# Optimization experiments

Measured on AMD Instinct MI355X. Metric: run time of the kernel, lower is better.

Reference implementation:

```python
import jax, jax.numpy as jnp
import numpy as np

MEM = 2048

def _linear_params(key, scale):
    kw, kb = jax.random.split(key)
    W = jax.random.uniform(kw, (MEM, MEM), jnp.float32, -scale, scale)
    b = jax.random.uniform(kb, (MEM,), jnp.float32, -scale, scale)
    return W, b

def setup_inputs() -> dict:
    key = jax.random.key(0)
    ks = jax.random.split(key, 18)
    scale = 1.0 / np.sqrt(MEM)
    inp = {
        'lc': jax.random.normal(ks[0], (1, MEM), jnp.float32),
        'lh': jax.random.normal(ks[1], (1, MEM), jnp.float32),
        'rc': jax.random.normal(ks[2], (1, MEM), jnp.float32),
        'rh': jax.random.normal(ks[3], (1, MEM), jnp.float32),
        'S': jax.random.normal(ks[4], (1, MEM), jnp.float32),
        'w': jax.random.normal(ks[5], (1, MEM), jnp.float32),
    }
    names = ['Wh', 'Us', 'ma', 'ilh', 'irh', 'lflh', 'lfrh', 'rflh', 'rfrh', 'ulh', 'urh']
    for i, n in enumerate(names):
        W, b = _linear_params(ks[6 + i], scale)
        inp[n + '_w'] = W
        inp[n + '_b'] = b
    return inp

def _lin(x, W, b):
    return x @ W.T + b

def reference(lc, lh, rc, rh, S, w,
              Wh_w, Wh_b, Us_w, Us_b, ma_w, ma_b,
              ilh_w, ilh_b, irh_w, irh_b,
              lflh_w, lflh_b, lfrh_w, lfrh_b,
              rflh_w, rflh_b, rfrh_w, rfrh_b,
              ulh_w, ulh_b, urh_w, urh_b):
    # attention scoring over the two children
    m_left = jnp.tanh(_lin(lh, Wh_w, Wh_b) + _lin(S, Us_w, Us_b)).squeeze()   # [MEM]
    m_right = jnp.tanh(_lin(rh, Wh_w, Wh_b) + _lin(S, Us_w, Us_b)).squeeze()  # [MEM]
    exp_left = w @ m_left[:, None]    # [1,1]
    exp_right = w @ m_right[:, None]  # [1,1]
    denom = exp_left + exp_right
    left_alpha = exp_left / denom
    right_alpha = exp_right / denom
    # attention-weighted child hidden states
    la = jnp.tanh(_lin(left_alpha * lh, ma_w, ma_b))   # [1,MEM]
    ra = jnp.tanh(_lin(right_alpha * rh, ma_w, ma_b))  # [1,MEM]
    # tree-LSTM gates
    i = jax.nn.sigmoid(_lin(la, ilh_w, ilh_b) + _lin(ra, irh_w, irh_b))
    lf = jax.nn.sigmoid(_lin(la, lflh_w, lflh_b) + _lin(ra, lfrh_w, lfrh_b))
    rf = jax.nn.sigmoid(_lin(la, rflh_w, rflh_b) + _lin(ra, rfrh_w, rfrh_b))
    update = jnp.tanh(_lin(la, ulh_w, ulh_b) + _lin(ra, urh_w, urh_b))
    c = i * update + lf * lc + rf * rc
    h = jnp.tanh(c)
    return (c, h)
```

## Files before the change

### kernel.cpp

```cpp
#include <hip/hip_runtime.h>
#include <hip/hip_bf16.h>
#include <math.h>

#define MEM 2048
#define NT  256
#define NF4 (MEM / 4)

__device__ __forceinline__ float dot4(float4 a, float4 b) {
    return a.x * b.x + a.y * b.y + a.z * b.z + a.w * b.w;
}

__device__ __forceinline__ float wave_reduce(float v) {
#pragma unroll
    for (int off = 32; off > 0; off >>= 1)
        v += __shfl_down(v, off, 64);
    return v;
}

__device__ __forceinline__ float sigmoidf_(float x) {
    return 1.0f / (1.0f + expf(-x));
}

__global__ __launch_bounds__(NT) void
k1_score(const float* __restrict__ lh, const float* __restrict__ rh,
         const float* __restrict__ S,  const float* __restrict__ w,
         const float* __restrict__ Wh_w, const float* __restrict__ Wh_b,
         const float* __restrict__ Us_w, const float* __restrict__ Us_b,
         const float* __restrict__ ma_w,
         float* __restrict__ pl, float* __restrict__ pr,
         float* __restrict__ wml, float* __restrict__ wmr)
{
    __shared__ float s_red[4][5];

    const int t   = threadIdx.x;
    const int row = blockIdx.x;

    const float4* __restrict__ wh4 = (const float4*)(Wh_w + (size_t)row * MEM);
    const float4* __restrict__ us4 = (const float4*)(Us_w + (size_t)row * MEM);
    const float4* __restrict__ ma4 = (const float4*)(ma_w + (size_t)row * MEM);
    const float4* __restrict__ l4  = (const float4*)lh;
    const float4* __restrict__ r4  = (const float4*)rh;
    const float4* __restrict__ s4  = (const float4*)S;

    float awl = 0.f, awr = 0.f, aus = 0.f, aml = 0.f, amr = 0.f;
#pragma unroll
    for (int h = 0; h < 2; ++h) {
        const int i = t + h * NT;
        const float4 a  = wh4[i];
        const float4 u  = us4[i];
        const float4 m  = ma4[i];
        const float4 xl = l4[i];
        const float4 xr = r4[i];
        const float4 xs = s4[i];
        awl += dot4(a, xl);
        awr += dot4(a, xr);
        aus += dot4(u, xs);
        aml += dot4(m, xl);
        amr += dot4(m, xr);
    }
    awl = wave_reduce(awl);
    awr = wave_reduce(awr);
    aus = wave_reduce(aus);
    aml = wave_reduce(aml);
    amr = wave_reduce(amr);

    const int wv = t >> 6, ln = t & 63;
    if (ln == 0) {
        s_red[wv][0] = awl; s_red[wv][1] = awr; s_red[wv][2] = aus;
        s_red[wv][3] = aml; s_red[wv][4] = amr;
    }
    __syncthreads();
    if (t == 0) {
        float r0 = 0.f, r1 = 0.f, r2 = 0.f, r3 = 0.f, r4v = 0.f;
#pragma unroll
        for (int k = 0; k < 4; ++k) {
            r0 += s_red[k][0]; r1 += s_red[k][1]; r2 += s_red[k][2];
            r3 += s_red[k][3]; r4v += s_red[k][4];
        }
        const float us = r2 + Us_b[row];
        const float ml = tanhf(r0 + Wh_b[row] + us);
        const float mr = tanhf(r1 + Wh_b[row] + us);
        pl[row] = r3;
        pr[row] = r4v;
        const float wj = w[row];
        wml[row] = wj * ml;
        wmr[row] = wj * mr;
    }
}

__global__ __launch_bounds__(NT) void
k2_gates(const float* __restrict__ lc, const float* __restrict__ rc,
         const float* __restrict__ pl, const float* __restrict__ pr,
         const float* __restrict__ wml, const float* __restrict__ wmr,
         const float* __restrict__ ma_b,
         const float* __restrict__ ilh_w,  const float* __restrict__ ilh_b,
         const float* __restrict__ irh_w,  const float* __restrict__ irh_b,
         const float* __restrict__ lflh_w, const float* __restrict__ lflh_b,
         const float* __restrict__ lfrh_w, const float* __restrict__ lfrh_b,
         const float* __restrict__ rflh_w, const float* __restrict__ rflh_b,
         const float* __restrict__ rfrh_w, const float* __restrict__ rfrh_b,
         const float* __restrict__ ulh_w,  const float* __restrict__ ulh_b,
         const float* __restrict__ urh_w,  const float* __restrict__ urh_b,
         float* __restrict__ out)
{
    __shared__ __align__(16) float s_la[MEM];
    __shared__ __align__(16) float s_ra[MEM];
    __shared__ float s_red[4][4];
    __shared__ float s_al[2];

    const int t   = threadIdx.x;
    const int wv  = t >> 6, ln = t & 63;
    const int row = blockIdx.x;

    {
        const float4* __restrict__ wl4 = (const float4*)wml;
        const float4* __restrict__ wr4 = (const float4*)wmr;
        const float4 a0 = wl4[t], a1 = wl4[t + NT];
        const float4 b0 = wr4[t], b1 = wr4[t + NT];
        float el = a0.x + a0.y + a0.z + a0.w + a1.x + a1.y + a1.z + a1.w;
        float er = b0.x + b0.y + b0.z + b0.w + b1.x + b1.y + b1.z + b1.w;
        el = wave_reduce(el);
        er = wave_reduce(er);
        if (ln == 0) { s_red[wv][0] = el; s_red[wv][1] = er; }
    }
    __syncthreads();
    if (t == 0) {
        const float el = s_red[0][0] + s_red[1][0] + s_red[2][0] + s_red[3][0];
        const float er = s_red[0][1] + s_red[1][1] + s_red[2][1] + s_red[3][1];
        const float d  = el + er;
        s_al[0] = el / d;
        s_al[1] = er / d;
    }
    __syncthreads();
    const float al = s_al[0];
    const float ar = s_al[1];

    {
        const float4* __restrict__ p4 = (const float4*)pl;
        const float4* __restrict__ q4 = (const float4*)pr;
        const float4* __restrict__ b4 = (const float4*)ma_b;
        float4* sla4 = (float4*)s_la;
        float4* sra4 = (float4*)s_ra;
#pragma unroll
        for (int h = 0; h < 2; ++h) {
            const int i = t + h * NT;
            const float4 p = p4[i];
            const float4 q = q4[i];
            const float4 b = b4[i];
            float4 la, ra;
            la.x = tanhf(al * p.x + b.x); ra.x = tanhf(ar * q.x + b.x);
            la.y = tanhf(al * p.y + b.y); ra.y = tanhf(ar * q.y + b.y);
            la.z = tanhf(al * p.z + b.z); ra.z = tanhf(ar * q.z + b.z);
            la.w = tanhf(al * p.w + b.w); ra.w = tanhf(ar * q.w + b.w);
            sla4[i] = la;
            sra4[i] = ra;
        }
    }
    __syncthreads();

    const size_t off = (size_t)row * MEM;
    const float4* __restrict__ il4  = (const float4*)(ilh_w  + off);
    const float4* __restrict__ ir4  = (const float4*)(irh_w  + off);
    const float4* __restrict__ lfl4 = (const float4*)(lflh_w + off);
    const float4* __restrict__ lfr4 = (const float4*)(lfrh_w + off);
    const float4* __restrict__ rfl4 = (const float4*)(rflh_w + off);
    const float4* __restrict__ rfr4 = (const float4*)(rfrh_w + off);
    const float4* __restrict__ ul4  = (const float4*)(ulh_w  + off);
    const float4* __restrict__ ur4  = (const float4*)(urh_w  + off);
    const float4* sla4 = (const float4*)s_la;
    const float4* sra4 = (const float4*)s_ra;

    float gi = 0.f, glf = 0.f, grf = 0.f, gu = 0.f;
#pragma unroll
    for (int h = 0; h < 2; ++h) {
        const int i = t + h * NT;
        const float4 w0 = il4[i];
        const float4 w1 = ir4[i];
        const float4 w2 = lfl4[i];
        const float4 w3 = lfr4[i];
        const float4 w4 = rfl4[i];
        const float4 w5 = rfr4[i];
        const float4 w6 = ul4[i];
        const float4 w7 = ur4[i];
        const float4 xa = sla4[i];
        const float4 xb = sra4[i];
        gi  += dot4(w0, xa) + dot4(w1, xb);
        glf += dot4(w2, xa) + dot4(w3, xb);
        grf += dot4(w4, xa) + dot4(w5, xb);
        gu  += dot4(w6, xa) + dot4(w7, xb);
    }
    gi  = wave_reduce(gi);
    glf = wave_reduce(glf);
    grf = wave_reduce(grf);
    gu  = wave_reduce(gu);
    if (ln == 0) {
        s_red[wv][0] = gi; s_red[wv][1] = glf; s_red[wv][2] = grf; s_red[wv][3] = gu;
    }
    __syncthreads();
    if (t == 0) {
        float r0 = 0.f, r1 = 0.f, r2 = 0.f, r3 = 0.f;
#pragma unroll
        for (int k = 0; k < 4; ++k) {
            r0 += s_red[k][0]; r1 += s_red[k][1];
            r2 += s_red[k][2]; r3 += s_red[k][3];
        }
        const float ig  = sigmoidf_(r0 + ilh_b[row]  + irh_b[row]);
        const float lfg = sigmoidf_(r1 + lflh_b[row] + lfrh_b[row]);
        const float rfg = sigmoidf_(r2 + rflh_b[row] + rfrh_b[row]);
        const float ug  = tanhf(r3 + ulh_b[row] + urh_b[row]);
        const float c   = ig * ug + lfg * lc[row] + rfg * rc[row];
        out[row]       = c;
        out[MEM + row] = tanhf(c);
    }
}

extern "C" void kernel_launch(void* const* d_in, const int* in_sizes, int n_in,
                              void* d_out, int out_size, void* d_ws, size_t ws_size,
                              hipStream_t stream) {
    const float* lc = (const float*)d_in[0];
    const float* lh = (const float*)d_in[1];
    const float* rc = (const float*)d_in[2];
    const float* rh = (const float*)d_in[3];
    const float* S  = (const float*)d_in[4];
    const float* w  = (const float*)d_in[5];
    const float* Wh_w   = (const float*)d_in[6];   const float* Wh_b   = (const float*)d_in[7];
    const float* Us_w   = (const float*)d_in[8];   const float* Us_b   = (const float*)d_in[9];
    const float* ma_w   = (const float*)d_in[10];  const float* ma_b   = (const float*)d_in[11];
    const float* ilh_w  = (const float*)d_in[12];  const float* ilh_b  = (const float*)d_in[13];
    const float* irh_w  = (const float*)d_in[14];  const float* irh_b  = (const float*)d_in[15];
    const float* lflh_w = (const float*)d_in[16];  const float* lflh_b = (const float*)d_in[17];
    const float* lfrh_w = (const float*)d_in[18];  const float* lfrh_b = (const float*)d_in[19];
    const float* rflh_w = (const float*)d_in[20];  const float* rflh_b = (const float*)d_in[21];
    const float* rfrh_w = (const float*)d_in[22];  const float* rfrh_b = (const float*)d_in[23];
    const float* ulh_w  = (const float*)d_in[24];  const float* ulh_b  = (const float*)d_in[25];
    const float* urh_w  = (const float*)d_in[26];  const float* urh_b  = (const float*)d_in[27];

    float* out = (float*)d_out;
    float* ws  = (float*)d_ws;
    float* pl  = ws;
    float* pr  = ws + MEM;
    float* wml = ws + 2 * MEM;
    float* wmr = ws + 3 * MEM;

    k1_score<<<MEM, NT, 0, stream>>>(lh, rh, S, w, Wh_w, Wh_b, Us_w, Us_b,
                                     ma_w, pl, pr, wml, wmr);

    k2_gates<<<MEM, NT, 0, stream>>>(lc, rc, pl, pr, wml, wmr, ma_b,
                                     ilh_w, ilh_b, irh_w, irh_b,
                                     lflh_w, lflh_b, lfrh_w, lfrh_b,
                                     rflh_w, rflh_b, rfrh_w, rfrh_b,
                                     ulh_w, ulh_b, urh_w, urh_b, out);
}
```

Baseline: 244.0 us.

## Split GEMVs into per-matrix slab kernels with wave-per-two-rows mapping

Replaces the two row-per-block kernels with four kernels. Two slab GEMV kernels give each matrix its own grid dimension and assign two rows per wave, staging the input vector in shared memory. A single-block kernel now computes the attention alphas and la/ra once instead of recomputing them in every block of the gate kernel, and a final elementwise kernel combines the gates. This is meant to cut redundant per-block work and spread the weight streaming across more independent blocks, at the cost of two extra launches and a serial single-block step.

```diff
diff --git a/kernel.cpp b/kernel.cpp
--- a/kernel.cpp
+++ b/kernel.cpp
@@ -3,8 +3,7 @@
 #include <math.h>
 
 #define MEM 2048
-#define NT  256
-#define NF4 (MEM / 4)
+#define NF4 512
 
 __device__ __forceinline__ float dot4(float4 a, float4 b) {
     return a.x * b.x + a.y * b.y + a.z * b.z + a.w * b.w;
@@ -21,197 +20,179 @@
     return 1.0f / (1.0f + expf(-x));
 }
 
-__global__ __launch_bounds__(NT) void
-k1_score(const float* __restrict__ lh, const float* __restrict__ rh,
-         const float* __restrict__ S,  const float* __restrict__ w,
-         const float* __restrict__ Wh_w, const float* __restrict__ Wh_b,
-         const float* __restrict__ Us_w, const float* __restrict__ Us_b,
-         const float* __restrict__ ma_w,
-         float* __restrict__ pl, float* __restrict__ pr,
-         float* __restrict__ wml, float* __restrict__ wmr)
-{
-    __shared__ float s_red[4][5];
-
-    const int t   = threadIdx.x;
-    const int row = blockIdx.x;
-
-    const float4* __restrict__ wh4 = (const float4*)(Wh_w + (size_t)row * MEM);
-    const float4* __restrict__ us4 = (const float4*)(Us_w + (size_t)row * MEM);
-    const float4* __restrict__ ma4 = (const float4*)(ma_w + (size_t)row * MEM);
-    const float4* __restrict__ l4  = (const float4*)lh;
-    const float4* __restrict__ r4  = (const float4*)rh;
-    const float4* __restrict__ s4  = (const float4*)S;
-
-    float awl = 0.f, awr = 0.f, aus = 0.f, aml = 0.f, amr = 0.f;
-#pragma unroll
-    for (int h = 0; h < 2; ++h) {
-        const int i = t + h * NT;
-        const float4 a  = wh4[i];
-        const float4 u  = us4[i];
-        const float4 m  = ma4[i];
-        const float4 xl = l4[i];
-        const float4 xr = r4[i];
-        const float4 xs = s4[i];
-        awl += dot4(a, xl);
-        awr += dot4(a, xr);
-        aus += dot4(u, xs);
-        aml += dot4(m, xl);
-        amr += dot4(m, xr);
-    }
-    awl = wave_reduce(awl);
-    awr = wave_reduce(awr);
-    aus = wave_reduce(aus);
-    aml = wave_reduce(aml);
-    amr = wave_reduce(amr);
+
+__global__ __launch_bounds__(256) void
+k1_slab(const float* __restrict__ lh, const float* __restrict__ rh,
+        const float* __restrict__ S,
+        const float* __restrict__ Wh_w, const float* __restrict__ Us_w,
+        const float* __restrict__ ma_w,
+        float* __restrict__ ws)
+{
+    __shared__ __align__(16) float s_x1[MEM];
+    __shared__ __align__(16) float s_x2[MEM];
+
+    const int t  = threadIdx.x;
+    const int m  = blockIdx.y;
+    const int rg = blockIdx.x;
+
+    const float* W  = (m == 0) ? Wh_w : (m == 1) ? Us_w : ma_w;
+    const float* x1 = (m == 1) ? S : lh;
+    const float* x2 = (m == 1) ? S : rh;
+
+    {
+        const float4* a4 = (const float4*)x1;
+        const float4* b4 = (const float4*)x2;
+        float4* s14 = (float4*)s_x1;
+        float4* s24 = (float4*)s_x2;
+        for (int i = t; i < NF4; i += 256) { s14[i] = a4[i]; s24[i] = b4[i]; }
+    }
+    __syncthreads();
 
     const int wv = t >> 6, ln = t & 63;
+    const int row0 = rg * 8 + wv * 2;
+
+    const float4* __restrict__ w0 = (const float4*)(W + (size_t)row0 * MEM);
+    const float4* __restrict__ w1 = w0 + NF4;
+    const float4* sx1 = (const float4*)s_x1;
+    const float4* sx2 = (const float4*)s_x2;
+
+    float a00 = 0.f, a01 = 0.f, a10 = 0.f, a11 = 0.f;
+#pragma unroll
+    for (int i = 0; i < 8; ++i) {
+        const int idx = i * 64 + ln;
+        const float4 wa = w0[idx];
+        const float4 wb = w1[idx];
+        const float4 p  = sx1[idx];
+        const float4 q  = sx2[idx];
+        a00 += dot4(wa, p); a01 += dot4(wa, q);
+        a10 += dot4(wb, p); a11 += dot4(wb, q);
+    }
+    a00 = wave_reduce(a00); a01 = wave_reduce(a01);
+    a10 = wave_reduce(a10); a11 = wave_reduce(a11);
+
     if (ln == 0) {
-        s_red[wv][0] = awl; s_red[wv][1] = awr; s_red[wv][2] = aus;
-        s_red[wv][3] = aml; s_red[wv][4] = amr;
-    }
+        if (m == 0) {
+            ws[row0] = a00; ws[row0 + 1] = a10;
+            ws[MEM + row0] = a01; ws[MEM + row0 + 1] = a11;
+        } else if (m == 1) {
+            ws[2 * MEM + row0] = a00; ws[2 * MEM + row0 + 1] = a10;
+        } else {
+            ws[3 * MEM + row0] = a00; ws[3 * MEM + row0 + 1] = a10;
+            ws[4 * MEM + row0] = a01; ws[4 * MEM + row0 + 1] = a11;
+        }
+    }
+}
+
+__global__ __launch_bounds__(1024) void
+k_mid(const float* __restrict__ w, const float* __restrict__ Wh_b,
+      const float* __restrict__ Us_b, const float* __restrict__ ma_b,
+      float* __restrict__ ws)
+{
+    __shared__ float s_red[16][2];
+    __shared__ float s_al[2];
+
+    const int t = threadIdx.x;
+    float el = 0.f, er = 0.f;
+    for (int j = t; j < MEM; j += 1024) {
+        const float us = ws[2 * MEM + j] + Us_b[j];
+        const float bb = Wh_b[j] + us;
+        const float ml = tanhf(ws[j] + bb);
+        const float mr = tanhf(ws[MEM + j] + bb);
+        const float wj = w[j];
+        el += wj * ml; er += wj * mr;
+    }
+    el = wave_reduce(el);
+    er = wave_reduce(er);
+    const int wv = t >> 6, ln = t & 63;
+    if (ln == 0) { s_red[wv][0] = el; s_red[wv][1] = er; }
     __syncthreads();
     if (t == 0) {
-        float r0 = 0.f, r1 = 0.f, r2 = 0.f, r3 = 0.f, r4v = 0.f;
-#pragma unroll
-        for (int k = 0; k < 4; ++k) {
-            r0 += s_red[k][0]; r1 += s_red[k][1]; r2 += s_red[k][2];
-            r3 += s_red[k][3]; r4v += s_red[k][4];
-        }
-        const float us = r2 + Us_b[row];
-        const float ml = tanhf(r0 + Wh_b[row] + us);
-        const float mr = tanhf(r1 + Wh_b[row] + us);
-        pl[row] = r3;
-        pr[row] = r4v;
-        const float wj = w[row];
-        wml[row] = wj * ml;
-        wmr[row] = wj * mr;
-    }
-}
-
-__global__ __launch_bounds__(NT) void
-k2_gates(const float* __restrict__ lc, const float* __restrict__ rc,
-         const float* __restrict__ pl, const float* __restrict__ pr,
-         const float* __restrict__ wml, const float* __restrict__ wmr,
-         const float* __restrict__ ma_b,
-         const float* __restrict__ ilh_w,  const float* __restrict__ ilh_b,
-         const float* __restrict__ irh_w,  const float* __restrict__ irh_b,
-         const float* __restrict__ lflh_w, const float* __restrict__ lflh_b,
-         const float* __restrict__ lfrh_w, const float* __restrict__ lfrh_b,
-         const float* __restrict__ rflh_w, const float* __restrict__ rflh_b,
-         const float* __restrict__ rfrh_w, const float* __restrict__ rfrh_b,
-         const float* __restrict__ ulh_w,  const float* __restrict__ ulh_b,
-         const float* __restrict__ urh_w,  const float* __restrict__ urh_b,
-         float* __restrict__ out)
-{
-    __shared__ __align__(16) float s_la[MEM];
-    __shared__ __align__(16) float s_ra[MEM];
-    __shared__ float s_red[4][4];
-    __shared__ float s_al[2];
-
-    const int t   = threadIdx.x;
-    const int wv  = t >> 6, ln = t & 63;
-    const int row = blockIdx.x;
-
-    {
-        const float4* __restrict__ wl4 = (const float4*)wml;
-        const float4* __restrict__ wr4 = (const float4*)wmr;
-        const float4 a0 = wl4[t], a1 = wl4[t + NT];
-        const float4 b0 = wr4[t], b1 = wr4[t + NT];
-        float el = a0.x + a0.y + a0.z + a0.w + a1.x + a1.y + a1.z + a1.w;
-        float er = b0.x + b0.y + b0.z + b0.w + b1.x + b1.y + b1.z + b1.w;
-        el = wave_reduce(el);
-        er = wave_reduce(er);
-        if (ln == 0) { s_red[wv][0] = el; s_red[wv][1] = er; }
-    }
-    __syncthreads();
-    if (t == 0) {
-        const float el = s_red[0][0] + s_red[1][0] + s_red[2][0] + s_red[3][0];
-        const float er = s_red[0][1] + s_red[1][1] + s_red[2][1] + s_red[3][1];
-        const float d  = el + er;
-        s_al[0] = el / d;
-        s_al[1] = er / d;
+        float e0 = 0.f, e1 = 0.f;
+#pragma unroll
+        for (int k = 0; k < 16; ++k) { e0 += s_red[k][0]; e1 += s_red[k][1]; }
+        const float d = e0 + e1;
+        s_al[0] = e0 / d;
+        s_al[1] = e1 / d;
     }
     __syncthreads();
     const float al = s_al[0];
     const float ar = s_al[1];
+    for (int j = t; j < MEM; j += 1024) {
+        const float mb = ma_b[j];
+        const float la = tanhf(al * ws[3 * MEM + j] + mb);
+        const float ra = tanhf(ar * ws[4 * MEM + j] + mb);
+        ws[j] = la;
+        ws[MEM + j] = ra;
+    }
+}
+
+__global__ __launch_bounds__(256) void
+k2_slab(const float* __restrict__ ilh_w,  const float* __restrict__ irh_w,
+        const float* __restrict__ lflh_w, const float* __restrict__ lfrh_w,
+        const float* __restrict__ rflh_w, const float* __restrict__ rfrh_w,
+        const float* __restrict__ ulh_w,  const float* __restrict__ urh_w,
+        float* __restrict__ ws)
+{
+    __shared__ __align__(16) float s_x[MEM];
+
+    const int t  = threadIdx.x;
+    const int m  = blockIdx.y;
+    const int rg = blockIdx.x;
+
+    const float* Wt[8] = {ilh_w, irh_w, lflh_w, lfrh_w, rflh_w, rfrh_w, ulh_w, urh_w};
+    const float* W = Wt[m];
+    const float* x = ws + (size_t)(m & 1) * MEM;
 
     {
-        const float4* __restrict__ p4 = (const float4*)pl;
-        const float4* __restrict__ q4 = (const float4*)pr;
-        const float4* __restrict__ b4 = (const float4*)ma_b;
-        float4* sla4 = (float4*)s_la;
-        float4* sra4 = (float4*)s_ra;
-#pragma unroll
-        for (int h = 0; h < 2; ++h) {
-            const int i = t + h * NT;
-            const float4 p = p4[i];
-            const float4 q = q4[i];
-            const float4 b = b4[i];
-            float4 la, ra;
-            la.x = tanhf(al * p.x + b.x); ra.x = tanhf(ar * q.x + b.x);
-            la.y = tanhf(al * p.y + b.y); ra.y = tanhf(ar * q.y + b.y);
-            la.z = tanhf(al * p.z + b.z); ra.z = tanhf(ar * q.z + b.z);
-            la.w = tanhf(al * p.w + b.w); ra.w = tanhf(ar * q.w + b.w);
-            sla4[i] = la;
-            sra4[i] = ra;
-        }
-    }
-    __syncthreads();
-
-    const size_t off = (size_t)row * MEM;
-    const float4* __restrict__ il4  = (const float4*)(ilh_w  + off);
-    const float4* __restrict__ ir4  = (const float4*)(irh_w  + off);
-    const float4* __restrict__ lfl4 = (const float4*)(lflh_w + off);
-    const float4* __restrict__ lfr4 = (const float4*)(lfrh_w + off);
-    const float4* __restrict__ rfl4 = (const float4*)(rflh_w + off);
-    const float4* __restrict__ rfr4 = (const float4*)(rfrh_w + off);
-    const float4* __restrict__ ul4  = (const float4*)(ulh_w  + off);
-    const float4* __restrict__ ur4  = (const float4*)(urh_w  + off);
-    const float4* sla4 = (const float4*)s_la;
-    const float4* sra4 = (const float4*)s_ra;
-
-    float gi = 0.f, glf = 0.f, grf = 0.f, gu = 0.f;
-#pragma unroll
-    for (int h = 0; h < 2; ++h) {
-        const int i = t + h * NT;
-        const float4 w0 = il4[i];
-        const float4 w1 = ir4[i];
-        const float4 w2 = lfl4[i];
-        const float4 w3 = lfr4[i];
-        const float4 w4 = rfl4[i];
-        const float4 w5 = rfr4[i];
-        const float4 w6 = ul4[i];
-        const float4 w7 = ur4[i];
-        const float4 xa = sla4[i];
-        const float4 xb = sra4[i];
-        gi  += dot4(w0, xa) + dot4(w1, xb);
-        glf += dot4(w2, xa) + dot4(w3, xb);
-        grf += dot4(w4, xa) + dot4(w5, xb);
-        gu  += dot4(w6, xa) + dot4(w7, xb);
-    }
-    gi  = wave_reduce(gi);
-    glf = wave_reduce(glf);
-    grf = wave_reduce(grf);
-    gu  = wave_reduce(gu);
+        const float4* x4 = (const float4*)x;
+        float4* s4 = (float4*)s_x;
+        for (int i = t; i < NF4; i += 256) s4[i] = x4[i];
+    }
+    __syncthreads();
+
+    const int wv = t >> 6, ln = t & 63;
+    const int row0 = rg * 8 + wv * 2;
+
+    const float4* __restrict__ w0 = (const float4*)(W + (size_t)row0 * MEM);
+    const float4* __restrict__ w1 = w0 + NF4;
+    const float4* sx = (const float4*)s_x;
+
+    float a0 = 0.f, a1 = 0.f;
+#pragma unroll
+    for (int i = 0; i < 8; ++i) {
+        const int idx = i * 64 + ln;
+        const float4 wa = w0[idx];
+        const float4 wb = w1[idx];
+        const float4 xv = sx[idx];
+        a0 += dot4(wa, xv);
+        a1 += dot4(wb, xv);
+    }
+    a0 = wave_reduce(a0);
+    a1 = wave_reduce(a1);
     if (ln == 0) {
-        s_red[wv][0] = gi; s_red[wv][1] = glf; s_red[wv][2] = grf; s_red[wv][3] = gu;
-    }
-    __syncthreads();
-    if (t == 0) {
-        float r0 = 0.f, r1 = 0.f, r2 = 0.f, r3 = 0.f;
-#pragma unroll
-        for (int k = 0; k < 4; ++k) {
-            r0 += s_red[k][0]; r1 += s_red[k][1];
-            r2 += s_red[k][2]; r3 += s_red[k][3];
-        }
-        const float ig  = sigmoidf_(r0 + ilh_b[row]  + irh_b[row]);
-        const float lfg = sigmoidf_(r1 + lflh_b[row] + lfrh_b[row]);
-        const float rfg = sigmoidf_(r2 + rflh_b[row] + rfrh_b[row]);
-        const float ug  = tanhf(r3 + ulh_b[row] + urh_b[row]);
-        const float c   = ig * ug + lfg * lc[row] + rfg * rc[row];
-        out[row]       = c;
-        out[MEM + row] = tanhf(c);
-    }
+        float* p = ws + (size_t)(2 + m) * MEM;
+        p[row0]     = a0;
+        p[row0 + 1] = a1;
+    }
+}
+
+__global__ __launch_bounds__(256) void
+k3_combine(const float* __restrict__ lc, const float* __restrict__ rc,
+           const float* __restrict__ ilh_b,  const float* __restrict__ irh_b,
+           const float* __restrict__ lflh_b, const float* __restrict__ lfrh_b,
+           const float* __restrict__ rflh_b, const float* __restrict__ rfrh_b,
+           const float* __restrict__ ulh_b,  const float* __restrict__ urh_b,
+           const float* __restrict__ ws, float* __restrict__ out)
+{
+    const int j = blockIdx.x * 256 + threadIdx.x;
+    const float* P = ws + 2 * MEM;
+    const float gi = sigmoidf_(P[j]           + P[MEM + j]     + ilh_b[j]  + irh_b[j]);
+    const float lf = sigmoidf_(P[2 * MEM + j] + P[3 * MEM + j] + lflh_b[j] + lfrh_b[j]);
+    const float rf = sigmoidf_(P[4 * MEM + j] + P[5 * MEM + j] + rflh_b[j] + rfrh_b[j]);
+    const float u  = tanhf(    P[6 * MEM + j] + P[7 * MEM + j] + ulh_b[j]  + urh_b[j]);
+    const float c  = gi * u + lf * lc[j] + rf * rc[j];
+    out[j]       = c;
+    out[MEM + j] = tanhf(c);
 }
 
 extern "C" void kernel_launch(void* const* d_in, const int* in_sizes, int n_in,
@@ -237,17 +218,16 @@
 
     float* out = (float*)d_out;
     float* ws  = (float*)d_ws;
-    float* pl  = ws;
-    float* pr  = ws + MEM;
-    float* wml = ws + 2 * MEM;
-    float* wmr = ws + 3 * MEM;
-
-    k1_score<<<MEM, NT, 0, stream>>>(lh, rh, S, w, Wh_w, Wh_b, Us_w, Us_b,
-                                     ma_w, pl, pr, wml, wmr);
-
-    k2_gates<<<MEM, NT, 0, stream>>>(lc, rc, pl, pr, wml, wmr, ma_b,
-                                     ilh_w, ilh_b, irh_w, irh_b,
-                                     lflh_w, lflh_b, lfrh_w, lfrh_b,
-                                     rflh_w, rflh_b, rfrh_w, rfrh_b,
-                                     ulh_w, ulh_b, urh_w, urh_b, out);
-}
+
+    dim3 g1(256, 3);
+    k1_slab<<<g1, 256, 0, stream>>>(lh, rh, S, Wh_w, Us_w, ma_w, ws);
+
+    k_mid<<<1, 1024, 0, stream>>>(w, Wh_b, Us_b, ma_b, ws);
+
+    dim3 g2(256, 8);
+    k2_slab<<<g2, 256, 0, stream>>>(ilh_w, irh_w, lflh_w, lfrh_w,
+                                    rflh_w, rfrh_w, ulh_w, urh_w, ws);
+
+    k3_combine<<<8, 256, 0, stream>>>(lc, rc, ilh_b, irh_b, lflh_b, lfrh_b,
+                                      rflh_b, rfrh_b, ulh_b, urh_b, ws, out);
+}
```

After: 251.3 us. 3.0% more time.
